# Kernel optimization log

Hardware: AMD Instinct MI355X
Metric: run time of the kernel (lower is better)

## Reference

```python
import jax, jax.numpy as jnp
import numpy as np
from jax import lax

EPS = 1e-5

def conv2d(x, w, groups=1, pad=0):
    return lax.conv_general_dilated(
        x, w, window_strides=(1, 1), padding=[(pad, pad), (pad, pad)],
        dimension_numbers=('NCHW', 'OIHW', 'NCHW'), feature_group_count=groups)

def setup_inputs() -> dict:
    key = jax.random.key(0)
    ks = jax.random.split(key, 10)
    B, C, H, W = 8, 64, 128, 128
    s = 0.05
    f32 = jnp.float32
    return {
        'x': jax.random.normal(ks[0], (B, C, H, W), f32),
        # key_embed: Conv2d(64,64,3,groups=8,bias=False) -> weight [64, 64/8, 3, 3]
        'w_key': jax.random.normal(ks[1], (64, 8, 3, 3), f32) * s,
        # embed[0]: Conv2d(128,32,1,groups=2,bias=False) -> [32, 128/2, 1, 1]
        'w_e1': jax.random.normal(ks[2], (32, 64, 1, 1), f32) * s,
        # embed[2]: Conv2d(32,72,1,groups=2,bias=True) -> [72, 32/2, 1, 1]
        'w_e2': jax.random.normal(ks[3], (72, 16, 1, 1), f32) * s,
        'b_e2': jax.random.normal(ks[4], (72,), f32) * s,
        # GroupNorm(num_groups=8, num_channels=72) affine params
        'gn_w': jnp.ones((72,), f32),
        'gn_b': jnp.zeros((72,), f32),
        # conv1x1: Conv2d(64,64,1,groups=2,bias=False) -> [64, 32, 1, 1]
        'w_c1': jax.random.normal(ks[5], (64, 32, 1, 1), f32) * s,
        # conv_du: Conv2d(64,4,1,bias=False), Conv2d(4,64,1,bias=False)
        'w_du1': jax.random.normal(ks[6], (4, 64, 1, 1), f32) * s,
        'w_du2': jax.random.normal(ks[7], (64, 4, 1, 1), f32) * s,
    }

def reference(x, w_key, w_e1, w_e2, b_e2, gn_w, gn_b, w_c1, w_du1, w_du2):
    B, C, H, W = x.shape  # C == 64
    KK = 9                # kernel_size^2
    # key embedding: grouped 3x3 conv + ReLU
    k = jax.nn.relu(conv2d(x, w_key, groups=8, pad=1))
    # interleave x and k along channels: view of [B,64,2,H,W] -> [B,128,H,W]
    qk = jnp.stack([x, k], axis=2).reshape(B, 2 * C, H, W)
    # dynamic kernel generation (embed)
    w = jax.nn.relu(conv2d(qk, w_e1, groups=2))
    w = conv2d(w, w_e2, groups=2) + b_e2[None, :, None, None]  # [B,72,H,W]
    # GroupNorm(8, 72): normalize over (channels-in-group, H, W)
    wg = w.reshape(B, 8, 9, H, W)
    m = wg.mean(axis=(2, 3, 4), keepdims=True)
    v = wg.var(axis=(2, 3, 4), keepdims=True)
    w = ((wg - m) * lax.rsqrt(v + EPS)).reshape(B, 72, H, W)
    w = w * gn_w[None, :, None, None] + gn_b[None, :, None, None]
    # per-pixel kernels: [B*2, 4, 9, H, W]
    w = w.reshape(B * 2, 4, KK, H, W)
    # value path
    xv = conv2d(x, w_c1, groups=2).reshape(B * 2, 32, H, W)
    # unfold 3x3 patches with zero padding 1 -> [B*2, 32, 9, H, W]
    xp = jnp.pad(xv, ((0, 0), (0, 0), (1, 1), (1, 1)))
    patches = jnp.stack(
        [xp[:, :, i:i + H, j:j + W] for i in range(3) for j in range(3)], axis=2)
    # share_planes=8: 8 channels share each kernel -> [B*2, 4, 8, 9, H, W]
    patches = patches.reshape(B * 2, 4, 8, KK, H, W)
    out = jnp.einsum('bgckhw,bgkhw->bgchw', patches, w)  # local conv
    out = out.reshape(B, C, H, W)
    # channel attention
    y = out.mean(axis=(2, 3))                 # [B, 64]
    y = jax.nn.relu(y @ w_du1[:, :, 0, 0].T)  # [B, 4]
    y = jax.nn.sigmoid(y @ w_du2[:, :, 0, 0].T)  # [B, 64]
    return out * y[:, :, None, None]
```

## Files before the change

kernel.cpp:

```cpp
#include <hip/hip_runtime.h>
#include <math.h>

#define Hd 128
#define Wd 128
#define HW 16384

__device__ __forceinline__ float wred(float v) {
  #pragma unroll
  for (int o = 32; o > 0; o >>= 1) v += __shfl_down(v, o, 64);
  return v;
}

__global__ __launch_bounds__(256) void k_fused(const float* __restrict__ x,
                                               const float* __restrict__ wkey,
                                               const float* __restrict__ we1,
                                               const float* __restrict__ we2,
                                               const float* __restrict__ be2,
                                               const float* __restrict__ wc1,
                                               float* __restrict__ xv,
                                               float* __restrict__ wpre,
                                               float* __restrict__ spart) {
  __shared__ float xt[8][18][24];
  __shared__ float sred2[4][8];
  const int tid = threadIdx.x;
  const int tx = tid & 15, ty = tid >> 4;
  const int b = blockIdx.y, s = blockIdx.z;
  const int h0 = (blockIdx.x >> 3) * 16, w0 = (blockIdx.x & 7) * 16;
  const int p = ((h0 + ty) << 7) + (w0 + tx);
  float xc[32], kc[32];
  for (int g = 0; g < 4; ++g) {
    for (int i = tid; i < 8 * 324; i += 256) {
      int ch = i / 324, r = i - ch * 324;
      int yy = r / 18, xx = r - yy * 18;
      int gh = h0 + yy - 1, gw = w0 + xx - 1;
      float v = 0.f;
      if (gh >= 0 && gh < Hd && gw >= 0 && gw < Wd)
        v = x[((long)(b * 64 + 32 * s + 8 * g + ch) << 14) + (gh << 7) + gw];
      xt[ch][yy][xx] = v;
    }
    __syncthreads();
    float kacc[8] = {0.f, 0.f, 0.f, 0.f, 0.f, 0.f, 0.f, 0.f};
    const float* wg = wkey + (4 * s + g) * 576;
    #pragma unroll
    for (int ich = 0; ich < 8; ++ich) {
      float nb[9];
      #pragma unroll
      for (int rr = 0; rr < 3; ++rr)
        #pragma unroll
        for (int cc = 0; cc < 3; ++cc)
          nb[rr * 3 + cc] = xt[ich][ty + rr][tx + cc];
      xc[8 * g + ich] = nb[4];
      #pragma unroll
      for (int oc = 0; oc < 8; ++oc) {
        const float* wr = wg + oc * 72 + ich * 9;
        #pragma unroll
        for (int k9 = 0; k9 < 9; ++k9) kacc[oc] += wr[k9] * nb[k9];
      }
    }
    #pragma unroll
    for (int oc = 0; oc < 8; ++oc) kc[8 * g + oc] = fmaxf(kacc[oc], 0.f);
    __syncthreads();
  }
  float* xvp = xv + ((long)((s * 8 + b) * HW + p)) * 32;
  #pragma unroll
  for (int o4 = 0; o4 < 8; ++o4) {
    float va[4];
    #pragma unroll
    for (int oo = 0; oo < 4; ++oo) {
      const float* wr = wc1 + (32 * s + 4 * o4 + oo) * 32;
      float a = 0.f;
      #pragma unroll
      for (int j = 0; j < 32; ++j) a += wr[j] * xc[j];
      va[oo] = a;
    }
    ((float4*)xvp)[o4] = make_float4(va[0], va[1], va[2], va[3]);
  }
  float w1a[16];
  #pragma unroll
  for (int o = 0; o < 16; ++o) {
    const float* wr = we1 + (16 * s + o) * 64;
    float a = 0.f;
    #pragma unroll
    for (int j = 0; j < 32; ++j) a += wr[2 * j] * xc[j] + wr[2 * j + 1] * kc[j];
    w1a[o] = fmaxf(a, 0.f);
  }
  float* wpp = wpre + ((long)((s * 8 + b) * HW + p)) * 36;
  #pragma unroll
  for (int gl = 0; gl < 4; ++gl) {
    float lgs = 0.f, lgq = 0.f;
    #pragma unroll
    for (int kk = 0; kk < 9; ++kk) {
      const int oc2 = 36 * s + gl * 9 + kk;
      const float* wr = we2 + oc2 * 16;
      float a = be2[oc2];
      #pragma unroll
      for (int ic = 0; ic < 16; ++ic) a += wr[ic] * w1a[ic];
      wpp[gl * 9 + kk] = a;
      lgs += a;
      lgq += a * a;
    }
    float r1 = wred(lgs), r2 = wred(lgq);
    if ((tid & 63) == 0) {
      sred2[tid >> 6][2 * gl] = r1;
      sred2[tid >> 6][2 * gl + 1] = r2;
    }
  }
  __syncthreads();
  if (tid < 8) {
    float a = sred2[0][tid] + sred2[1][tid] + sred2[2][tid] + sred2[3][tid];
    spart[blockIdx.x * 128 + b * 16 + s * 8 + tid] = a;
  }
}

__global__ __launch_bounds__(256) void k_local(const float* __restrict__ xv,
                                               const float* __restrict__ wpre,
                                               const float* __restrict__ spart,
                                               const float* __restrict__ gnw,
                                               const float* __restrict__ gnb,
                                               float* __restrict__ out,
                                               float* __restrict__ part) {
  __shared__ float xt[8][34][24];
  __shared__ float sminv[2];
  const int tid = threadIdx.x;
  const int tx = tid & 15, ty = tid >> 4;
  const int z = blockIdx.z;
  const int b2 = z >> 2, g = z & 3;
  const int t = b2 & 1, b = b2 >> 1;
  const int gg = 4 * t + g;
  const int h0 = blockIdx.y * 32, w0 = blockIdx.x * 16;
  for (int i = tid; i < 612; i += 256) {
    int yy = i / 34, xx = i - yy * 34;
    yy = i / 18; xx = i - yy * 18;
    int gh = h0 + yy - 1, gw = w0 + xx - 1;
    float4 v0 = make_float4(0.f, 0.f, 0.f, 0.f), v1 = v0;
    if (gh >= 0 && gh < Hd && gw >= 0 && gw < Wd) {
      const float4* src = (const float4*)(xv +
          ((long)((t * 8 + b) * HW) + (gh << 7) + gw) * 32 + 8 * g);
      v0 = src[0];
      v1 = src[1];
    }
    xt[0][yy][xx] = v0.x; xt[1][yy][xx] = v0.y; xt[2][yy][xx] = v0.z; xt[3][yy][xx] = v0.w;
    xt[4][yy][xx] = v1.x; xt[5][yy][xx] = v1.y; xt[6][yy][xx] = v1.z; xt[7][yy][xx] = v1.w;
  }
  if (tid < 64) {
    const float* sp = spart + tid * 128 + (b * 8 + gg) * 2;
    float sv = sp[0], qv = sp[1];
    #pragma unroll
    for (int o = 32; o > 0; o >>= 1) {
      sv += __shfl_down(sv, o, 64);
      qv += __shfl_down(qv, o, 64);
    }
    if (tid == 0) {
      const float N = 9.f * (float)HW;
      float mm = sv / N;
      float var = qv / N - mm * mm;
      sminv[0] = mm;
      sminv[1] = rsqrtf(var + 1e-5f);
    }
  }
  __syncthreads();
  const float m = sminv[0];
  const float inv = sminv[1];
  const int p0 = ((h0 + 2 * ty) << 7) + (w0 + tx);
  const int p1 = p0 + 128;
  const float* w0p = wpre + ((long)((t * 8 + b) * HW + p0)) * 36 + 9 * g;
  const float* w1p = wpre + ((long)((t * 8 + b) * HW + p1)) * 36 + 9 * g;
  float wn0[9], wn1[9];
  #pragma unroll
  for (int kk = 0; kk < 9; ++kk) {
    const int ch72 = 36 * t + 9 * g + kk;
    const float sc = inv * gnw[ch72], sh = gnb[ch72] - m * inv * gnw[ch72];
    wn0[kk] = w0p[kk] * sc + sh;
    wn1[kk] = w1p[kk] * sc + sh;
  }
  const int prow = (blockIdx.y * 8 + blockIdx.x) * 4 + (tid >> 6);
  #pragma unroll
  for (int cc = 0; cc < 8; ++cc) {
    float nb[12];
    #pragma unroll
    for (int rr = 0; rr < 4; ++rr)
      #pragma unroll
      for (int ccol = 0; ccol < 3; ++ccol)
        nb[rr * 3 + ccol] = xt[cc][2 * ty + rr][tx + ccol];
    float o0 = 0.f, o1 = 0.f;
    #pragma unroll
    for (int dy = 0; dy < 3; ++dy)
      #pragma unroll
      for (int dx = 0; dx < 3; ++dx) {
        o0 += wn0[dy * 3 + dx] * nb[dy * 3 + dx];
        o1 += wn1[dy * 3 + dx] * nb[(dy + 1) * 3 + dx];
      }
    const int ch512 = b2 * 32 + g * 8 + cc;
    out[((long)ch512 << 14) + p0] = o0;
    out[((long)ch512 << 14) + p1] = o1;
    float os = wred(o0 + o1);
    if ((tid & 63) == 0) part[prow * 512 + ch512] = os;
  }
}

__global__ void k_ca(const float* __restrict__ part, const float* __restrict__ du1,
                     const float* __restrict__ du2, float* __restrict__ ys) {
  __shared__ float sy[8][64];
  __shared__ float sy4[8][4];
  const int tid = threadIdx.x;
  const int b = tid >> 6, c = tid & 63;
  float acc = 0.f;
  #pragma unroll 8
  for (int r = 0; r < 128; ++r) acc += part[r * 512 + tid];
  sy[b][c] = acc * (1.f / (float)HW);
  __syncthreads();
  if (tid < 32) {
    int bb = tid >> 2, j = tid & 3;
    float a = 0.f;
    for (int c2 = 0; c2 < 64; ++c2) a += sy[bb][c2] * du1[j * 64 + c2];
    sy4[bb][j] = fmaxf(a, 0.f);
  }
  __syncthreads();
  float z = 0.f;
  #pragma unroll
  for (int j = 0; j < 4; ++j) z += sy4[b][j] * du2[c * 4 + j];
  ys[tid] = 1.f / (1.f + expf(-z));
}

__global__ __launch_bounds__(256) void k_scale(float* __restrict__ out,
                                               const float* __restrict__ ys) {
  const long i4 = (long)blockIdx.x * 256 + threadIdx.x;
  const long e = i4 * 4;
  const int bc = (int)(e >> 14);
  const float s = ys[bc];
  float4* o = (float4*)out;
  float4 v = o[i4];
  v.x *= s; v.y *= s; v.z *= s; v.w *= s;
  o[i4] = v;
}

extern "C" void kernel_launch(void* const* d_in, const int* in_sizes, int n_in,
                              void* d_out, int out_size, void* d_ws, size_t ws_size,
                              hipStream_t stream) {
  const float* x    = (const float*)d_in[0];
  const float* wkey = (const float*)d_in[1];
  const float* we1  = (const float*)d_in[2];
  const float* we2  = (const float*)d_in[3];
  const float* be2  = (const float*)d_in[4];
  const float* gnw  = (const float*)d_in[5];
  const float* gnb  = (const float*)d_in[6];
  const float* wc1  = (const float*)d_in[7];
  const float* du1  = (const float*)d_in[8];
  const float* du2  = (const float*)d_in[9];
  float* out = (float*)d_out;
  float* ws = (float*)d_ws;

  float* xv   = ws;
  float* wpre = ws + 8388608;
  float* part = ws + 17825792;
  float* spart = part + 65536;
  float* ys   = spart + 8192;

  k_fused<<<dim3(64, 8, 2), 256, 0, stream>>>(x, wkey, we1, we2, be2, wc1, xv, wpre, spart);
  k_local<<<dim3(8, 4, 64), 256, 0, stream>>>(xv, wpre, spart, gnw, gnb, out, part);
  k_ca<<<1, 512, 0, stream>>>(part, du1, du2, ys);
  k_scale<<<8192, 256, 0, stream>>>(out, ys);
}
```

Before: 230.9 us.

## Store 16-channel hidden embed instead of 36 pre-norm kernel weights, recompute in local pass

The fused kernel now writes the 16-channel ReLU hidden activation in a planar layout instead of the 36 pre-GroupNorm kernel weights per pixel. The local-conv kernel rebuilds the 9 weights it needs per pixel from those 16 values with the second 1x1 conv, then applies GroupNorm. This cuts the intermediate buffer's write and read traffic. In exchange each of the 4 group blocks re-reads all 16 hidden channels and redoes 16x9 FMAs per pixel.

```diff
diff --git a/kernel.cpp b/kernel.cpp
--- a/kernel.cpp
+++ b/kernel.cpp
@@ -18,7 +18,7 @@
                                                const float* __restrict__ be2,
                                                const float* __restrict__ wc1,
                                                float* __restrict__ xv,
-                                               float* __restrict__ wpre,
+                                               float* __restrict__ w1out,
                                                float* __restrict__ spart) {
   __shared__ float xt[8][18][24];
   __shared__ float sred2[4][8];
@@ -83,8 +83,8 @@
     #pragma unroll
     for (int j = 0; j < 32; ++j) a += wr[2 * j] * xc[j] + wr[2 * j + 1] * kc[j];
     w1a[o] = fmaxf(a, 0.f);
-  }
-  float* wpp = wpre + ((long)((s * 8 + b) * HW + p)) * 36;
+    w1out[((long)((s * 16 + o) * 8 + b) << 14) + p] = w1a[o];
+  }
   #pragma unroll
   for (int gl = 0; gl < 4; ++gl) {
     float lgs = 0.f, lgq = 0.f;
@@ -95,7 +95,6 @@
       float a = be2[oc2];
       #pragma unroll
       for (int ic = 0; ic < 16; ++ic) a += wr[ic] * w1a[ic];
-      wpp[gl * 9 + kk] = a;
       lgs += a;
       lgq += a * a;
     }
@@ -113,7 +112,9 @@
 }
 
 __global__ __launch_bounds__(256) void k_local(const float* __restrict__ xv,
-                                               const float* __restrict__ wpre,
+                                               const float* __restrict__ w1in,
+                                               const float* __restrict__ we2,
+                                               const float* __restrict__ be2,
                                                const float* __restrict__ spart,
                                                const float* __restrict__ gnw,
                                                const float* __restrict__ gnb,
@@ -129,8 +130,7 @@
   const int gg = 4 * t + g;
   const int h0 = blockIdx.y * 32, w0 = blockIdx.x * 16;
   for (int i = tid; i < 612; i += 256) {
-    int yy = i / 34, xx = i - yy * 34;
-    yy = i / 18; xx = i - yy * 18;
+    int yy = i / 18, xx = i - yy * 18;
     int gh = h0 + yy - 1, gw = w0 + xx - 1;
     float4 v0 = make_float4(0.f, 0.f, 0.f, 0.f), v1 = v0;
     if (gh >= 0 && gh < Hd && gw >= 0 && gw < Wd) {
@@ -163,15 +163,35 @@
   const float inv = sminv[1];
   const int p0 = ((h0 + 2 * ty) << 7) + (w0 + tx);
   const int p1 = p0 + 128;
-  const float* w0p = wpre + ((long)((t * 8 + b) * HW + p0)) * 36 + 9 * g;
-  const float* w1p = wpre + ((long)((t * 8 + b) * HW + p1)) * 36 + 9 * g;
   float wn0[9], wn1[9];
-  #pragma unroll
-  for (int kk = 0; kk < 9; ++kk) {
-    const int ch72 = 36 * t + 9 * g + kk;
-    const float sc = inv * gnw[ch72], sh = gnb[ch72] - m * inv * gnw[ch72];
-    wn0[kk] = w0p[kk] * sc + sh;
-    wn1[kk] = w1p[kk] * sc + sh;
+  {
+    float v[16];
+    #pragma unroll
+    for (int o = 0; o < 16; ++o)
+      v[o] = w1in[((long)((t * 16 + o) * 8 + b) << 14) + p0];
+    #pragma unroll
+    for (int kk = 0; kk < 9; ++kk) {
+      const int ch72 = 36 * t + 9 * g + kk;
+      const float* wr = we2 + ch72 * 16;
+      float a = be2[ch72];
+      #pragma unroll
+      for (int ic = 0; ic < 16; ++ic) a += wr[ic] * v[ic];
+      const float sc = inv * gnw[ch72];
+      wn0[kk] = a * sc + (gnb[ch72] - m * sc);
+    }
+    #pragma unroll
+    for (int o = 0; o < 16; ++o)
+      v[o] = w1in[((long)((t * 16 + o) * 8 + b) << 14) + p1];
+    #pragma unroll
+    for (int kk = 0; kk < 9; ++kk) {
+      const int ch72 = 36 * t + 9 * g + kk;
+      const float* wr = we2 + ch72 * 16;
+      float a = be2[ch72];
+      #pragma unroll
+      for (int ic = 0; ic < 16; ++ic) a += wr[ic] * v[ic];
+      const float sc = inv * gnw[ch72];
+      wn1[kk] = a * sc + (gnb[ch72] - m * sc);
+    }
   }
   const int prow = (blockIdx.y * 8 + blockIdx.x) * 4 + (tid >> 6);
   #pragma unroll
@@ -251,13 +271,13 @@
   float* ws = (float*)d_ws;
 
   float* xv   = ws;
-  float* wpre = ws + 8388608;
-  float* part = ws + 17825792;
+  float* w1a  = ws + 8388608;
+  float* part = ws + 12582912;
   float* spart = part + 65536;
   float* ys   = spart + 8192;
 
-  k_fused<<<dim3(64, 8, 2), 256, 0, stream>>>(x, wkey, we1, we2, be2, wc1, xv, wpre, spart);
-  k_local<<<dim3(8, 4, 64), 256, 0, stream>>>(xv, wpre, spart, gnw, gnb, out, part);
+  k_fused<<<dim3(64, 8, 2), 256, 0, stream>>>(x, wkey, we1, we2, be2, wc1, xv, w1a, spart);
+  k_local<<<dim3(8, 4, 64), 256, 0, stream>>>(xv, w1a, we2, be2, spart, gnw, gnb, out, part);
   k_ca<<<1, 512, 0, stream>>>(part, du1, du2, ys);
   k_scale<<<8192, 256, 0, stream>>>(out, ys);
 }
```

After: 232.3 us. About the same (+0.6%).
